# Kernel optimization log

Hardware: AMD Instinct MI355X
Metric: run time of the kernel (lower is better)

## Reference

```python
import jax, jax.numpy as jnp
import numpy as np

NEG = float(-2**32 + 1)  # huge negative used by the original sign-based masking
EPS = 1e-8
NUM_BLOCKS = 3
NUM_HEADS = 1


def _mha(xq, xk, xv, Wq, bq, Wk, bk, Wv, bv):
    # manual QKV with ReLU, as in the torch module
    Q = jax.nn.relu(xq @ Wq + bq)   # [B, Lq, D]
    K = jax.nn.relu(xk @ Wk + bk)   # [B, Lk, D]
    V = jax.nn.relu(xv @ Wv + bv)
    B, Lq, D = Q.shape
    Lk = K.shape[1]
    dh = D // NUM_HEADS
    Qh = Q.reshape(B, Lq, NUM_HEADS, dh)
    Kh = K.reshape(B, Lk, NUM_HEADS, dh)
    Vh = V.reshape(B, Lk, NUM_HEADS, dh)
    scores = jnp.einsum('bqhd,bkhd->bhqk', Qh, Kh) / jnp.sqrt(jnp.float32(dh))
    # sign-based key padding mask (rows whose embedding-sum is exactly 0)
    key_mask0 = (jnp.sign(jnp.abs(jnp.sum(xk, axis=-1))) == 0.0).astype(scores.dtype)  # [B, Lk]
    cond = key_mask0[:, None, None, :]
    scores = NEG * cond + scores * (1.0 - cond)
    attn = jax.nn.softmax(scores, axis=-1)
    # post-softmax query mask
    qmask = jnp.sign(jnp.abs(jnp.sum(xq, axis=-1)))  # [B, Lq]
    attn = attn * qmask[:, None, :, None]
    out = jnp.einsum('bhqk,bkhd->bqhd', attn, Vh).reshape(B, Lq, D)
    return out + xq  # residual; note: the torch mha never applies its layernorm


def _layernorm(x, g, b):
    mu = jnp.mean(x, axis=-1, keepdims=True)
    var = jnp.mean(jnp.square(x - mu), axis=-1, keepdims=True)
    return (x - mu) / jnp.sqrt(var + EPS) * g + b


def _ffn(x, W1, b1, W2, b2, g, bln):
    h = jax.nn.relu(x @ W1 + b1) @ W2 + b2
    return _layernorm(h, g, bln) + x


def setup_inputs() -> dict:
    key = jax.random.key(0)
    ks = jax.random.split(key, 9)
    B, L, V, D, NB = 4096, 50, 50000, 200, NUM_BLOCKS
    tokens = jax.random.randint(ks[0], (B, L), 0, V)
    emb = jax.random.normal(ks[1], (V, D), dtype=jnp.float32) * 0.1
    emb = emb.at[0].set(0.0)  # padding token row -> triggers sign masks
    s = 1.0 / np.sqrt(D)
    Wq = jax.random.normal(ks[2], (NB, D, D), dtype=jnp.float32) * s
    Wk = jax.random.normal(ks[3], (NB, D, D), dtype=jnp.float32) * s
    Wv = jax.random.normal(ks[4], (NB, D, D), dtype=jnp.float32) * s
    W1 = jax.random.normal(ks[5], (NB, D, D), dtype=jnp.float32) * s
    W2 = jax.random.normal(ks[6], (NB, D, D), dtype=jnp.float32) * s
    z = jnp.zeros((NB, D), dtype=jnp.float32)
    return dict(tokens=tokens, emb=emb,
                Wq=Wq, bq=z, Wk=Wk, bk=z, Wv=Wv, bv=z,
                W1=W1, b1=z, W2=W2, b2=z,
                ln_g=jnp.ones((NB, D), dtype=jnp.float32), ln_b=z)


def reference(tokens, emb, Wq, bq, Wk, bk, Wv, bv, W1, b1, W2, b2, ln_g, ln_b):
    x = emb[tokens]  # [B, L, D]
    for i in range(NUM_BLOCKS):
        x = _mha(x, x, x, Wq[i], bq[i], Wk[i], bk[i], Wv[i], bv[i])
        x = _ffn(x, W1[i], b1[i], W2[i], b2[i], ln_g[i], ln_b[i])
    return x
```

## Files before the change

### kernel.cpp

```cpp
#include <hip/hip_runtime.h>
#include <hip/hip_bf16.h>
#include <math.h>

#define LQ 50
#define DD 200
#define NBLK 3
#define NT 512

#define KT 7
#define NTL 14
#define MAT_U (KT * NTL * 128)

#define APS 408
#define VTS 72
#define PS  136
#define SS  66

#define NEGC (-4294967295.0f)
#define SCALE 0.07071067811865475f

typedef __attribute__((ext_vector_type(4))) float f32x4;
typedef __attribute__((ext_vector_type(8))) short s16x8;

__device__ __forceinline__ unsigned short bf16_rne(float x) {
  unsigned u = __float_as_uint(x);
  unsigned r = u + 0x7FFF + ((u >> 16) & 1);
  return (unsigned short)(r >> 16);
}
__device__ __forceinline__ float bf16_f(unsigned short h) {
  return __uint_as_float((unsigned)h << 16);
}

__device__ __forceinline__ void splitf(float x, short& h, short& l) {
  __hip_bfloat16 bh = __float2bfloat16(x);
  float hf = __bfloat162float(bh);
  __hip_bfloat16 bl = __float2bfloat16(x - hf);
  h = (short)__builtin_bit_cast(unsigned short, bh);
  l = (short)__builtin_bit_cast(unsigned short, bl);
}
__device__ __forceinline__ unsigned short bfbits(float x) {
  __hip_bfloat16 bh = __float2bfloat16(x);
  return __builtin_bit_cast(unsigned short, bh);
}
__device__ __forceinline__ float joinf(short h, short l) {
  return __bfloat162float(__builtin_bit_cast(__hip_bfloat16, (unsigned short)h)) +
         __bfloat162float(__builtin_bit_cast(__hip_bfloat16, (unsigned short)l));
}

__device__ __forceinline__ float wave_sum(float v) {
  #pragma unroll
  for (int off = 32; off > 0; off >>= 1) v += __shfl_xor(v, off, 64);
  return v;
}
__device__ __forceinline__ float wave_max(float v) {
  #pragma unroll
  for (int off = 32; off > 0; off >>= 1) v = fmaxf(v, __shfl_xor(v, off, 64));
  return v;
}

__global__ __launch_bounds__(64)
void swizzle_w(const float* __restrict__ Wq, const float* __restrict__ Wk,
               const float* __restrict__ Wv, const float* __restrict__ W1,
               const float* __restrict__ W2, unsigned short* __restrict__ wbuf)
{
  int t = blockIdx.x;
  int nt = t % NTL; t /= NTL;
  int kt = t % KT;  t /= KT;
  int mat = t;
  int layer = mat / 5, which = mat % 5;
  const float* W;
  switch (which) {
    case 0: W = Wq; break;
    case 1: W = Wk; break;
    case 2: W = Wv; break;
    case 3: W = W1; break;
    default: W = W2; break;
  }
  W += (size_t)layer * DD * DD;

  const int l = threadIdx.x;
  const int g = l >> 4, c = l & 15;
  const int n = nt * 16 + c;
  s16x8 vh, vl;
  #pragma unroll
  for (int j = 0; j < 8; ++j) {
    int k = kt * 32 + g * 8 + j;
    float w = (k < DD && n < DD) ? W[k * DD + n] : 0.0f;
    unsigned short h = bf16_rne(w);
    unsigned short lo = bf16_rne(w - bf16_f(h));
    vh[j] = (short)h;
    vl[j] = (short)lo;
  }
  size_t base = ((size_t)(mat * KT * NTL + kt * NTL + nt) * 2) * 512 + l * 8;
  *(s16x8*)(wbuf + base)       = vh;
  *(s16x8*)(wbuf + base + 512) = vl;
}

template <int MODE>
__device__ __forceinline__ void big_matmul(
    const short* __restrict__ srcp, const s16x8* __restrict__ wt,
    const float* __restrict__ bias, short* __restrict__ dstp,
    float* __restrict__ dstf, int wv, int lane)
{
  const int g = lane >> 4, c = lane & 15;
  const int n1 = wv, n2 = wv + 8;
  const bool has2 = (n2 < 13);

  const short* arow[4];
  #pragma unroll
  for (int m = 0; m < 4; ++m) {
    int r = m * 16 + c;
    if (r >= LQ) r = 0;
    arow[m] = srcp + r * APS;
  }

  f32x4 acc0[4], acc1[4];
  #pragma unroll
  for (int m = 0; m < 4; ++m) { acc0[m] = (f32x4)0.f; acc1[m] = (f32x4)0.f; }

  const s16x8* p1 = wt + n1 * 128 + lane;
  s16x8 b1h = p1[0], b1l = p1[64];
  s16x8 b2h = (s16x8)0, b2l = (s16x8)0;
  if (has2) { const s16x8* p2 = wt + n2 * 128 + lane; b2h = p2[0]; b2l = p2[64]; }

  #pragma unroll 1
  for (int kt = 0; kt < KT; ++kt) {
    s16x8 x1h = (s16x8)0, x1l = (s16x8)0, x2h = (s16x8)0, x2l = (s16x8)0;
    if (kt + 1 < KT) {
      const s16x8* q1 = wt + ((kt + 1) * NTL + n1) * 128 + lane;
      x1h = q1[0]; x1l = q1[64];
      if (has2) {
        const s16x8* q2 = wt + ((kt + 1) * NTL + n2) * 128 + lane;
        x2h = q2[0]; x2l = q2[64];
      }
    }
    const int ch = kt * 4 + g;
    s16x8 ah[4], al[4];
    if (ch < 25) {
      #pragma unroll
      for (int m = 0; m < 4; ++m) {
        const short* ap = arow[m] + ch * 16;
        ah[m] = *(const s16x8*)ap;
        al[m] = *(const s16x8*)(ap + 8);
      }
    } else {
      #pragma unroll
      for (int m = 0; m < 4; ++m) { ah[m] = (s16x8)0; al[m] = (s16x8)0; }
    }
    if (MODE == 0) {
      #pragma unroll
      for (int m = 0; m < 4; ++m) {
        acc0[m] = __builtin_amdgcn_mfma_f32_16x16x32_bf16(b1h, ah[m], acc0[m], 0, 0, 0);
        acc0[m] = __builtin_amdgcn_mfma_f32_16x16x32_bf16(b1h, al[m], acc0[m], 0, 0, 0);
        acc0[m] = __builtin_amdgcn_mfma_f32_16x16x32_bf16(b1l, ah[m], acc0[m], 0, 0, 0);
      }
      if (has2) {
        #pragma unroll
        for (int m = 0; m < 4; ++m) {
          acc1[m] = __builtin_amdgcn_mfma_f32_16x16x32_bf16(b2h, ah[m], acc1[m], 0, 0, 0);
          acc1[m] = __builtin_amdgcn_mfma_f32_16x16x32_bf16(b2h, al[m], acc1[m], 0, 0, 0);
          acc1[m] = __builtin_amdgcn_mfma_f32_16x16x32_bf16(b2l, ah[m], acc1[m], 0, 0, 0);
        }
      }
    } else {
      #pragma unroll
      for (int m = 0; m < 4; ++m) {
        acc0[m] = __builtin_amdgcn_mfma_f32_16x16x32_bf16(ah[m], b1h, acc0[m], 0, 0, 0);
        acc0[m] = __builtin_amdgcn_mfma_f32_16x16x32_bf16(al[m], b1h, acc0[m], 0, 0, 0);
        acc0[m] = __builtin_amdgcn_mfma_f32_16x16x32_bf16(ah[m], b1l, acc0[m], 0, 0, 0);
      }
      if (has2) {
        #pragma unroll
        for (int m = 0; m < 4; ++m) {
          acc1[m] = __builtin_amdgcn_mfma_f32_16x16x32_bf16(ah[m], b2h, acc1[m], 0, 0, 0);
          acc1[m] = __builtin_amdgcn_mfma_f32_16x16x32_bf16(al[m], b2h, acc1[m], 0, 0, 0);
          acc1[m] = __builtin_amdgcn_mfma_f32_16x16x32_bf16(ah[m], b2l, acc1[m], 0, 0, 0);
        }
      }
    }
    b1h = x1h; b1l = x1l; b2h = x2h; b2l = x2l;
  }

  if (MODE == 0) {
    #pragma unroll
    for (int t = 0; t < 2; ++t) {
      const int nt = t ? n2 : n1;
      if (nt < 13) {
        const int nb = nt * 16 + g * 4;
        if (nb + 3 < DD) {
          float4 bv = *(const float4*)(bias + nb);
          #pragma unroll
          for (int m = 0; m < 4; ++m) {
            const int r = m * 16 + c;
            if (r < LQ) {
              const f32x4 ac = t ? acc1[m] : acc0[m];
              float v0 = fmaxf(ac[0] + bv.x, 0.f);
              float v1 = fmaxf(ac[1] + bv.y, 0.f);
              float v2 = fmaxf(ac[2] + bv.z, 0.f);
              float v3 = fmaxf(ac[3] + bv.w, 0.f);
              short h0, l0, h1, l1, h2, l2, h3, l3;
              splitf(v0, h0, l0); splitf(v1, h1, l1);
              splitf(v2, h2, l2); splitf(v3, h3, l3);
              uint2 ph, pl;
              ph.x = (unsigned short)h0 | ((unsigned)(unsigned short)h1 << 16);
              ph.y = (unsigned short)h2 | ((unsigned)(unsigned short)h3 << 16);
              pl.x = (unsigned short)l0 | ((unsigned)(unsigned short)l1 << 16);
              pl.y = (unsigned short)l2 | ((unsigned)(unsigned short)l3 << 16);
              short* base = dstp + r * APS + (nb >> 3) * 16 + (nb & 7);
              *(uint2*)base = ph;
              *(uint2*)(base + 8) = pl;
            }
          }
        }
      }
    }
  } else {
    #pragma unroll
    for (int t = 0; t < 2; ++t) {
      const int nt = t ? n2 : n1;
      const int col = nt * 16 + c;
      if (col < DD) {
        const float bv = bias[col];
        #pragma unroll
        for (int m = 0; m < 4; ++m) {
          const int rb = m * 16 + g * 4;
          if (MODE == 1) {
            float vv[4];
            #pragma unroll
            for (int q = 0; q < 4; ++q) {
              const int r = rb + q;
              float v = (t ? acc1[m][q] : acc0[m][q]) + bv;
              vv[q] = (r < LQ) ? fmaxf(v, 0.f) : 0.f;
            }
            unsigned u0 = (unsigned)bfbits(vv[0]) | ((unsigned)bfbits(vv[1]) << 16);
            unsigned u1 = (unsigned)bfbits(vv[2]) | ((unsigned)bfbits(vv[3]) << 16);
            uint2 pk; pk.x = u0; pk.y = u1;
            *(uint2*)(dstp + col * VTS + (rb >> 3) * 8 + (rb & 7)) = pk;
          } else {
            #pragma unroll
            for (int q = 0; q < 4; ++q) {
              const int r = rb + q;
              float v = (t ? acc1[m][q] : acc0[m][q]) + bv;
              if (r < LQ) dstf[r * DD + col] = v;
            }
          }
        }
      }
    }
  }
}

__global__ __launch_bounds__(NT)
void transformer_kernel(const int* __restrict__ tokens,
                        const float* __restrict__ emb,
                        const unsigned short* __restrict__ wbuf,
                        const float* __restrict__ bq, const float* __restrict__ bk,
                        const float* __restrict__ bv, const float* __restrict__ b1,
                        const float* __restrict__ b2,
                        const float* __restrict__ lng, const float* __restrict__ lnb,
                        float* __restrict__ out)
{
  __shared__ __align__(16) short xs_p[LQ * APS];
  __shared__ __align__(16) short q_p [LQ * APS];
  __shared__ __align__(16) short k_p [LQ * APS];
  __shared__ __align__(16) short vt_p[DD * VTS];
  __shared__ float rowsum[52];

  float* Sf   = (float*)q_p;
  short* Pp   = q_p + 8192;
  float* h2f  = (float*)k_p;

  const int b    = blockIdx.x;
  const int tid  = threadIdx.x;
  const int lane = tid & 63;
  const int wv   = tid >> 6;
  const int g    = lane >> 4, c = lane & 15;

  for (int o = tid; o < LQ * 25; o += NT) {
    int r = o / 25, ch = o % 25;
    int tok = tokens[b * LQ + r];
    const float* ep = emb + (size_t)tok * DD + ch * 8;
    float4 a0 = *(const float4*)ep;
    float4 a1 = *(const float4*)(ep + 4);
    float xv[8] = {a0.x, a0.y, a0.z, a0.w, a1.x, a1.y, a1.z, a1.w};
    s16x8 hh, ll;
    #pragma unroll
    for (int j = 0; j < 8; ++j) { short h, l; splitf(xv[j], h, l); hh[j] = h; ll[j] = l; }
    short* dp = xs_p + r * APS + ch * 16;
    *(s16x8*)dp = hh;
    *(s16x8*)(dp + 8) = ll;
  }
  __syncthreads();

  for (int layer = 0; layer < NBLK; ++layer) {
    const s16x8* wq  = (const s16x8*)wbuf + (size_t)(layer * 5 + 0) * MAT_U;
    const s16x8* wk  = (const s16x8*)wbuf + (size_t)(layer * 5 + 1) * MAT_U;
    const s16x8* wvv = (const s16x8*)wbuf + (size_t)(layer * 5 + 2) * MAT_U;
    const s16x8* w1  = (const s16x8*)wbuf + (size_t)(layer * 5 + 3) * MAT_U;
    const s16x8* w2  = (const s16x8*)wbuf + (size_t)(layer * 5 + 4) * MAT_U;
    const float* bql = bq + layer * DD;
    const float* bkl = bk + layer * DD;
    const float* bvl = bv + layer * DD;
    const float* b1l = b1 + layer * DD;
    const float* b2l = b2 + layer * DD;
    const float* gl  = lng + layer * DD;
    const float* bl  = lnb + layer * DD;

    for (int r = wv; r < LQ; r += 8) {
      float s = 0.f;
      #pragma unroll
      for (int t = 0; t < 4; ++t) {
        int cc = lane + 64 * t;
        if (cc < DD) {
          const short* p = xs_p + r * APS + (cc >> 3) * 16 + (cc & 7);
          s += joinf(p[0], p[8]);
        }
      }
      s = wave_sum(s);
      if (lane == 0) rowsum[r] = s;
    }

    big_matmul<0>(xs_p, wq,  bql, q_p,  nullptr, wv, lane);
    big_matmul<0>(xs_p, wk,  bkl, k_p,  nullptr, wv, lane);
    big_matmul<1>(xs_p, wvv, bvl, vt_p, nullptr, wv, lane);
    __syncthreads();

    f32x4 s0 = (f32x4)0.f, s1 = (f32x4)0.f;
    {
      const int mt = wv >> 1;
      const int nk0 = (wv & 1) * 2;
      int qr = mt * 16 + c;         if (qr >= LQ) qr = 0;
      int kj0 = nk0 * 16 + c;       if (kj0 >= LQ) kj0 = 0;
      int kj1 = (nk0 + 1) * 16 + c; if (kj1 >= LQ) kj1 = 0;
      const short* qrow = q_p + qr * APS;
      const short* k0r  = k_p + kj0 * APS;
      const short* k1r  = k_p + kj1 * APS;
      #pragma unroll 1
      for (int kt = 0; kt < KT; ++kt) {
        const int ch = kt * 4 + g;
        s16x8 qh = (s16x8)0, ql = (s16x8)0;
        s16x8 kh0 = (s16x8)0, kl0 = (s16x8)0, kh1 = (s16x8)0, kl1 = (s16x8)0;
        if (ch < 25) {
          qh  = *(const s16x8*)(qrow + ch * 16); ql  = *(const s16x8*)(qrow + ch * 16 + 8);
          kh0 = *(const s16x8*)(k0r + ch * 16);  kl0 = *(const s16x8*)(k0r + ch * 16 + 8);
          kh1 = *(const s16x8*)(k1r + ch * 16);  kl1 = *(const s16x8*)(k1r + ch * 16 + 8);
        }
        s0 = __builtin_amdgcn_mfma_f32_16x16x32_bf16(qh, kh0, s0, 0, 0, 0);
        s0 = __builtin_amdgcn_mfma_f32_16x16x32_bf16(ql, kh0, s0, 0, 0, 0);
        s0 = __builtin_amdgcn_mfma_f32_16x16x32_bf16(qh, kl0, s0, 0, 0, 0);
        s1 = __builtin_amdgcn_mfma_f32_16x16x32_bf16(qh, kh1, s1, 0, 0, 0);
        s1 = __builtin_amdgcn_mfma_f32_16x16x32_bf16(ql, kh1, s1, 0, 0, 0);
        s1 = __builtin_amdgcn_mfma_f32_16x16x32_bf16(qh, kl1, s1, 0, 0, 0);
      }
    }
    __syncthreads();

    {
      const int mt = wv >> 1;
      const int nk0 = (wv & 1) * 2;
      #pragma unroll
      for (int t = 0; t < 2; ++t) {
        const int j = (nk0 + t) * 16 + c;
        const f32x4 sa = t ? s1 : s0;
        const bool km = (j < LQ) && (rowsum[j] != 0.0f);
        #pragma unroll
        for (int q = 0; q < 4; ++q) {
          const int qi = mt * 16 + g * 4 + q;
          if (qi < LQ) Sf[qi * SS + j] = km ? sa[q] * SCALE : NEGC;
        }
      }
    }
    __syncthreads();

    for (int r = wv; r < LQ; r += 8) {
      float sm = -INFINITY;
      if (lane < LQ) sm = Sf[r * SS + lane];
      float m = wave_max(sm);
      float e = (lane < LQ) ? __expf(sm - m) : 0.0f;
      float ssum = wave_sum(e);
      float qm = (rowsum[r] == 0.0f) ? 0.0f : 1.0f;
      float a = e / ssum * qm;
      short h, l; splitf(a, h, l);
      short* pp = Pp + r * PS + (lane >> 3) * 16 + (lane & 7);
      pp[0] = h; pp[8] = l;
    }
    __syncthreads();

    {
      s16x8 pbh[4][2], pbl[4][2];
      #pragma unroll
      for (int nq = 0; nq < 4; ++nq) {
        int pr = nq * 16 + c; if (pr >= LQ) pr = 0;
        const short* pp = Pp + pr * PS;
        #pragma unroll
        for (int kt = 0; kt < 2; ++kt) {
          pbh[nq][kt] = *(const s16x8*)(pp + (kt * 4 + g) * 16);
          pbl[nq][kt] = *(const s16x8*)(pp + (kt * 4 + g) * 16 + 8);
        }
      }
      #pragma unroll
      for (int mi = 0; mi < 2; ++mi) {
        const int mt = wv + 8 * mi;
        if (mt < 13) {
          f32x4 pa[4];
          #pragma unroll
          for (int nq = 0; nq < 4; ++nq) pa[nq] = (f32x4)0.f;
          int vr = mt * 16 + c; if (vr >= DD) vr = 0;
          const short* vrow = vt_p + vr * VTS;
          #pragma unroll
          for (int kt = 0; kt < 2; ++kt) {
            s16x8 vh = *(const s16x8*)(vrow + (kt * 4 + g) * 8);
            #pragma unroll
            for (int nq = 0; nq < 4; ++nq) {
              pa[nq] = __builtin_amdgcn_mfma_f32_16x16x32_bf16(vh, pbh[nq][kt], pa[nq], 0, 0, 0);
              pa[nq] = __builtin_amdgcn_mfma_f32_16x16x32_bf16(vh, pbl[nq][kt], pa[nq], 0, 0, 0);
            }
          }
          const int d0 = mt * 16 + g * 4;
          if (d0 + 3 < DD) {
            #pragma unroll
            for (int nq = 0; nq < 4; ++nq) {
              const int qq = nq * 16 + c;
              if (qq < LQ) {
                short* base = xs_p + qq * APS + (d0 >> 3) * 16 + (d0 & 7);
                uint2 ph = *(const uint2*)base;
                uint2 pl = *(const uint2*)(base + 8);
                float f0 = joinf((short)(ph.x & 0xFFFF), (short)(pl.x & 0xFFFF)) + pa[nq][0];
                float f1 = joinf((short)(ph.x >> 16),    (short)(pl.x >> 16))    + pa[nq][1];
                float f2 = joinf((short)(ph.y & 0xFFFF), (short)(pl.y & 0xFFFF)) + pa[nq][2];
                float f3 = joinf((short)(ph.y >> 16),    (short)(pl.y >> 16))    + pa[nq][3];
                short h0, l0, h1, l1, h2, l2, h3, l3;
                splitf(f0, h0, l0); splitf(f1, h1, l1);
                splitf(f2, h2, l2); splitf(f3, h3, l3);
                ph.x = (unsigned short)h0 | ((unsigned)(unsigned short)h1 << 16);
                ph.y = (unsigned short)h2 | ((unsigned)(unsigned short)h3 << 16);
                pl.x = (unsigned short)l0 | ((unsigned)(unsigned short)l1 << 16);
                pl.y = (unsigned short)l2 | ((unsigned)(unsigned short)l3 << 16);
                *(uint2*)base = ph;
                *(uint2*)(base + 8) = pl;
              }
            }
          }
        }
      }
    }
    __syncthreads();

    big_matmul<0>(xs_p, w1, b1l, q_p, nullptr, wv, lane);
    __syncthreads();
    big_matmul<2>(q_p, w2, b2l, nullptr, h2f, wv, lane);
    __syncthreads();

    for (int r = wv; r < LQ; r += 8) {
      float hv[4];
      #pragma unroll
      for (int t = 0; t < 4; ++t) {
        int cc = lane + 64 * t;
        hv[t] = (cc < DD) ? h2f[r * DD + cc] : 0.f;
      }
      float mu = wave_sum(hv[0] + hv[1] + hv[2] + hv[3]) * (1.0f / 200.0f);
      float d0 = hv[0] - mu, d1 = hv[1] - mu, d2 = hv[2] - mu;
      float d3 = (lane + 192 < DD) ? (hv[3] - mu) : 0.f;
      float var = wave_sum(d0 * d0 + d1 * d1 + d2 * d2 + d3 * d3) * (1.0f / 200.0f);
      float inv = 1.0f / sqrtf(var + 1e-8f);
      float dd4[4] = {d0, d1, d2, d3};
      #pragma unroll
      for (int t = 0; t < 4; ++t) {
        int cc = lane + 64 * t;
        if (cc < DD) {
          short* hp = xs_p + r * APS + (cc >> 3) * 16 + (cc & 7);
          float nv = dd4[t] * inv * gl[cc] + bl[cc] + joinf(hp[0], hp[8]);
          short h, l; splitf(nv, h, l);
          hp[0] = h; hp[8] = l;
        }
      }
    }
    __syncthreads();
  }

  for (int o = tid; o < LQ * 25; o += NT) {
    int r = o / 25, ch = o % 25;
    const short* sp = xs_p + r * APS + ch * 16;
    s16x8 hh = *(const s16x8*)sp;
    s16x8 ll = *(const s16x8*)(sp + 8);
    float4 o0, o1;
    o0.x = joinf(hh[0], ll[0]); o0.y = joinf(hh[1], ll[1]);
    o0.z = joinf(hh[2], ll[2]); o0.w = joinf(hh[3], ll[3]);
    o1.x = joinf(hh[4], ll[4]); o1.y = joinf(hh[5], ll[5]);
    o1.z = joinf(hh[6], ll[6]); o1.w = joinf(hh[7], ll[7]);
    float* op = out + ((size_t)b * LQ + r) * DD + ch * 8;
    *(float4*)op = o0;
    *(float4*)(op + 4) = o1;
  }
}

extern "C" void kernel_launch(void* const* d_in, const int* in_sizes, int n_in,
                              void* d_out, int out_size, void* d_ws, size_t ws_size,
                              hipStream_t stream) {
  const int*   tokens = (const int*)  d_in[0];
  const float* emb    = (const float*)d_in[1];
  const float* Wq     = (const float*)d_in[2];
  const float* bq     = (const float*)d_in[3];
  const float* Wk     = (const float*)d_in[4];
  const float* bk     = (const float*)d_in[5];
  const float* Wv     = (const float*)d_in[6];
  const float* bv     = (const float*)d_in[7];
  const float* W1     = (const float*)d_in[8];
  const float* b1     = (const float*)d_in[9];
  const float* W2     = (const float*)d_in[10];
  const float* b2     = (const float*)d_in[11];
  const float* lng    = (const float*)d_in[12];
  const float* lnb    = (const float*)d_in[13];
  float* out = (float*)d_out;
  unsigned short* wbuf = (unsigned short*)d_ws;

  hipLaunchKernelGGL(swizzle_w, dim3(15 * KT * NTL), dim3(64), 0, stream,
                     Wq, Wk, Wv, W1, W2, wbuf);

  const int B = in_sizes[0] / LQ;
  hipLaunchKernelGGL(transformer_kernel, dim3(B), dim3(NT), 0, stream,
                     tokens, emb, wbuf, bq, bk, bv, b1, b2, lng, lnb, out);
}
```

Baseline: 1.887 ms.

## Double block to 16 waves, giving each wave one output tile

Raises the workgroup from 8 to 16 waves and remaps work so each wave owns a single 16-column tile in the projection matmuls, a single score tile in QK^T, and a single V tile in PV. Row loops for layernorm and softmax now stride by 16 waves. This shortens the per-wave critical path and exposes more parallelism per block. In exchange, 3 of 16 waves sit idle in the matmuls, the weight loads per wave are no longer shared across two tiles, and the larger block may cut blocks per CU or limit registers.

```diff
diff --git a/kernel.cpp b/kernel.cpp
--- a/kernel.cpp
+++ b/kernel.cpp
@@ -5,7 +5,8 @@
 #define LQ 50
 #define DD 200
 #define NBLK 3
-#define NT 512
+#define NT 1024
+#define NW 16
 
 #define KT 7
 #define NTL 14
@@ -102,9 +103,10 @@
     const float* __restrict__ bias, short* __restrict__ dstp,
     float* __restrict__ dstf, int wv, int lane)
 {
+  const bool act = (wv < 13);
+  if (!act) return;
   const int g = lane >> 4, c = lane & 15;
-  const int n1 = wv, n2 = wv + 8;
-  const bool has2 = (n2 < 13);
+  const int n1 = wv;
 
   const short* arow[4];
   #pragma unroll
@@ -114,25 +116,19 @@
     arow[m] = srcp + r * APS;
   }
 
-  f32x4 acc0[4], acc1[4];
+  f32x4 acc0[4];
   #pragma unroll
-  for (int m = 0; m < 4; ++m) { acc0[m] = (f32x4)0.f; acc1[m] = (f32x4)0.f; }
+  for (int m = 0; m < 4; ++m) acc0[m] = (f32x4)0.f;
 
   const s16x8* p1 = wt + n1 * 128 + lane;
   s16x8 b1h = p1[0], b1l = p1[64];
-  s16x8 b2h = (s16x8)0, b2l = (s16x8)0;
-  if (has2) { const s16x8* p2 = wt + n2 * 128 + lane; b2h = p2[0]; b2l = p2[64]; }
 
   #pragma unroll 1
   for (int kt = 0; kt < KT; ++kt) {
-    s16x8 x1h = (s16x8)0, x1l = (s16x8)0, x2h = (s16x8)0, x2l = (s16x8)0;
+    s16x8 x1h = (s16x8)0, x1l = (s16x8)0;
     if (kt + 1 < KT) {
       const s16x8* q1 = wt + ((kt + 1) * NTL + n1) * 128 + lane;
       x1h = q1[0]; x1l = q1[64];
-      if (has2) {
-        const s16x8* q2 = wt + ((kt + 1) * NTL + n2) * 128 + lane;
-        x2h = q2[0]; x2l = q2[64];
-      }
     }
     const int ch = kt * 4 + g;
     s16x8 ah[4], al[4];
@@ -154,14 +150,6 @@
         acc0[m] = __builtin_amdgcn_mfma_f32_16x16x32_bf16(b1h, al[m], acc0[m], 0, 0, 0);
         acc0[m] = __builtin_amdgcn_mfma_f32_16x16x32_bf16(b1l, ah[m], acc0[m], 0, 0, 0);
       }
-      if (has2) {
-        #pragma unroll
-        for (int m = 0; m < 4; ++m) {
-          acc1[m] = __builtin_amdgcn_mfma_f32_16x16x32_bf16(b2h, ah[m], acc1[m], 0, 0, 0);
-          acc1[m] = __builtin_amdgcn_mfma_f32_16x16x32_bf16(b2h, al[m], acc1[m], 0, 0, 0);
-          acc1[m] = __builtin_amdgcn_mfma_f32_16x16x32_bf16(b2l, ah[m], acc1[m], 0, 0, 0);
-        }
-      }
     } else {
       #pragma unroll
       for (int m = 0; m < 4; ++m) {
@@ -169,80 +157,62 @@
         acc0[m] = __builtin_amdgcn_mfma_f32_16x16x32_bf16(al[m], b1h, acc0[m], 0, 0, 0);
         acc0[m] = __builtin_amdgcn_mfma_f32_16x16x32_bf16(ah[m], b1l, acc0[m], 0, 0, 0);
       }
-      if (has2) {
-        #pragma unroll
-        for (int m = 0; m < 4; ++m) {
-          acc1[m] = __builtin_amdgcn_mfma_f32_16x16x32_bf16(ah[m], b2h, acc1[m], 0, 0, 0);
-          acc1[m] = __builtin_amdgcn_mfma_f32_16x16x32_bf16(al[m], b2h, acc1[m], 0, 0, 0);
-          acc1[m] = __builtin_amdgcn_mfma_f32_16x16x32_bf16(ah[m], b2l, acc1[m], 0, 0, 0);
-        }
-      }
-    }
-    b1h = x1h; b1l = x1l; b2h = x2h; b2l = x2l;
+    }
+    b1h = x1h; b1l = x1l;
   }
 
   if (MODE == 0) {
-    #pragma unroll
-    for (int t = 0; t < 2; ++t) {
-      const int nt = t ? n2 : n1;
-      if (nt < 13) {
-        const int nb = nt * 16 + g * 4;
-        if (nb + 3 < DD) {
-          float4 bv = *(const float4*)(bias + nb);
+    const int nb = n1 * 16 + g * 4;
+    if (nb + 3 < DD) {
+      float4 bv = *(const float4*)(bias + nb);
+      #pragma unroll
+      for (int m = 0; m < 4; ++m) {
+        const int r = m * 16 + c;
+        if (r < LQ) {
+          const f32x4 ac = acc0[m];
+          float v0 = fmaxf(ac[0] + bv.x, 0.f);
+          float v1 = fmaxf(ac[1] + bv.y, 0.f);
+          float v2 = fmaxf(ac[2] + bv.z, 0.f);
+          float v3 = fmaxf(ac[3] + bv.w, 0.f);
+          short h0, l0, h1, l1, h2, l2, h3, l3;
+          splitf(v0, h0, l0); splitf(v1, h1, l1);
+          splitf(v2, h2, l2); splitf(v3, h3, l3);
+          uint2 ph, pl;
+          ph.x = (unsigned short)h0 | ((unsigned)(unsigned short)h1 << 16);
+          ph.y = (unsigned short)h2 | ((unsigned)(unsigned short)h3 << 16);
+          pl.x = (unsigned short)l0 | ((unsigned)(unsigned short)l1 << 16);
+          pl.y = (unsigned short)l2 | ((unsigned)(unsigned short)l3 << 16);
+          short* base = dstp + r * APS + (nb >> 3) * 16 + (nb & 7);
+          *(uint2*)base = ph;
+          *(uint2*)(base + 8) = pl;
+        }
+      }
+    }
+  } else {
+    const int col = n1 * 16 + c;
+    if (col < DD) {
+      const float bv = bias[col];
+      #pragma unroll
+      for (int m = 0; m < 4; ++m) {
+        const int rb = m * 16 + g * 4;
+        if (MODE == 1) {
+          float vv[4];
           #pragma unroll
-          for (int m = 0; m < 4; ++m) {
-            const int r = m * 16 + c;
-            if (r < LQ) {
-              const f32x4 ac = t ? acc1[m] : acc0[m];
-              float v0 = fmaxf(ac[0] + bv.x, 0.f);
-              float v1 = fmaxf(ac[1] + bv.y, 0.f);
-              float v2 = fmaxf(ac[2] + bv.z, 0.f);
-              float v3 = fmaxf(ac[3] + bv.w, 0.f);
-              short h0, l0, h1, l1, h2, l2, h3, l3;
-              splitf(v0, h0, l0); splitf(v1, h1, l1);
-              splitf(v2, h2, l2); splitf(v3, h3, l3);
-              uint2 ph, pl;
-              ph.x = (unsigned short)h0 | ((unsigned)(unsigned short)h1 << 16);
-              ph.y = (unsigned short)h2 | ((unsigned)(unsigned short)h3 << 16);
-              pl.x = (unsigned short)l0 | ((unsigned)(unsigned short)l1 << 16);
-              pl.y = (unsigned short)l2 | ((unsigned)(unsigned short)l3 << 16);
-              short* base = dstp + r * APS + (nb >> 3) * 16 + (nb & 7);
-              *(uint2*)base = ph;
-              *(uint2*)(base + 8) = pl;
-            }
+          for (int q = 0; q < 4; ++q) {
+            const int r = rb + q;
+            float v = acc0[m][q] + bv;
+            vv[q] = (r < LQ) ? fmaxf(v, 0.f) : 0.f;
           }
-        }
-      }
-    }
-  } else {
-    #pragma unroll
-    for (int t = 0; t < 2; ++t) {
-      const int nt = t ? n2 : n1;
-      const int col = nt * 16 + c;
-      if (col < DD) {
-        const float bv = bias[col];
-        #pragma unroll
-        for (int m = 0; m < 4; ++m) {
-          const int rb = m * 16 + g * 4;
-          if (MODE == 1) {
-            float vv[4];
-            #pragma unroll
-            for (int q = 0; q < 4; ++q) {
-              const int r = rb + q;
-              float v = (t ? acc1[m][q] : acc0[m][q]) + bv;
-              vv[q] = (r < LQ) ? fmaxf(v, 0.f) : 0.f;
-            }
-            unsigned u0 = (unsigned)bfbits(vv[0]) | ((unsigned)bfbits(vv[1]) << 16);
-            unsigned u1 = (unsigned)bfbits(vv[2]) | ((unsigned)bfbits(vv[3]) << 16);
-            uint2 pk; pk.x = u0; pk.y = u1;
-            *(uint2*)(dstp + col * VTS + (rb >> 3) * 8 + (rb & 7)) = pk;
-          } else {
-            #pragma unroll
-            for (int q = 0; q < 4; ++q) {
-              const int r = rb + q;
-              float v = (t ? acc1[m][q] : acc0[m][q]) + bv;
-              if (r < LQ) dstf[r * DD + col] = v;
-            }
+          unsigned u0 = (unsigned)bfbits(vv[0]) | ((unsigned)bfbits(vv[1]) << 16);
+          unsigned u1 = (unsigned)bfbits(vv[2]) | ((unsigned)bfbits(vv[3]) << 16);
+          uint2 pk; pk.x = u0; pk.y = u1;
+          *(uint2*)(dstp + col * VTS + (rb >> 3) * 8 + (rb & 7)) = pk;
+        } else {
+          #pragma unroll
+          for (int q = 0; q < 4; ++q) {
+            const int r = rb + q;
+            float v = acc0[m][q] + bv;
+            if (r < LQ) dstf[r * DD + col] = v;
           }
         }
       }
@@ -306,7 +276,7 @@
     const float* gl  = lng + layer * DD;
     const float* bl  = lnb + layer * DD;
 
-    for (int r = wv; r < LQ; r += 8) {
+    for (int r = wv; r < LQ; r += NW) {
       float s = 0.f;
       #pragma unroll
       for (int t = 0; t < 4; ++t) {
@@ -325,54 +295,44 @@
     big_matmul<1>(xs_p, wvv, bvl, vt_p, nullptr, wv, lane);
     __syncthreads();
 
-    f32x4 s0 = (f32x4)0.f, s1 = (f32x4)0.f;
+    f32x4 s0 = (f32x4)0.f;
     {
-      const int mt = wv >> 1;
-      const int nk0 = (wv & 1) * 2;
-      int qr = mt * 16 + c;         if (qr >= LQ) qr = 0;
-      int kj0 = nk0 * 16 + c;       if (kj0 >= LQ) kj0 = 0;
-      int kj1 = (nk0 + 1) * 16 + c; if (kj1 >= LQ) kj1 = 0;
+      const int mt  = wv >> 2;
+      const int ntk = wv & 3;
+      int qr = mt * 16 + c;   if (qr >= LQ) qr = 0;
+      int kj = ntk * 16 + c;  if (kj >= LQ) kj = 0;
       const short* qrow = q_p + qr * APS;
-      const short* k0r  = k_p + kj0 * APS;
-      const short* k1r  = k_p + kj1 * APS;
+      const short* k0r  = k_p + kj * APS;
       #pragma unroll 1
       for (int kt = 0; kt < KT; ++kt) {
         const int ch = kt * 4 + g;
         s16x8 qh = (s16x8)0, ql = (s16x8)0;
-        s16x8 kh0 = (s16x8)0, kl0 = (s16x8)0, kh1 = (s16x8)0, kl1 = (s16x8)0;
+        s16x8 kh0 = (s16x8)0, kl0 = (s16x8)0;
         if (ch < 25) {
           qh  = *(const s16x8*)(qrow + ch * 16); ql  = *(const s16x8*)(qrow + ch * 16 + 8);
           kh0 = *(const s16x8*)(k0r + ch * 16);  kl0 = *(const s16x8*)(k0r + ch * 16 + 8);
-          kh1 = *(const s16x8*)(k1r + ch * 16);  kl1 = *(const s16x8*)(k1r + ch * 16 + 8);
         }
         s0 = __builtin_amdgcn_mfma_f32_16x16x32_bf16(qh, kh0, s0, 0, 0, 0);
         s0 = __builtin_amdgcn_mfma_f32_16x16x32_bf16(ql, kh0, s0, 0, 0, 0);
         s0 = __builtin_amdgcn_mfma_f32_16x16x32_bf16(qh, kl0, s0, 0, 0, 0);
-        s1 = __builtin_amdgcn_mfma_f32_16x16x32_bf16(qh, kh1, s1, 0, 0, 0);
-        s1 = __builtin_amdgcn_mfma_f32_16x16x32_bf16(ql, kh1, s1, 0, 0, 0);
-        s1 = __builtin_amdgcn_mfma_f32_16x16x32_bf16(qh, kl1, s1, 0, 0, 0);
       }
     }
     __syncthreads();
 
     {
-      const int mt = wv >> 1;
-      const int nk0 = (wv & 1) * 2;
-      #pragma unroll
-      for (int t = 0; t < 2; ++t) {
-        const int j = (nk0 + t) * 16 + c;
-        const f32x4 sa = t ? s1 : s0;
-        const bool km = (j < LQ) && (rowsum[j] != 0.0f);
-        #pragma unroll
-        for (int q = 0; q < 4; ++q) {
-          const int qi = mt * 16 + g * 4 + q;
-          if (qi < LQ) Sf[qi * SS + j] = km ? sa[q] * SCALE : NEGC;
-        }
-      }
-    }
-    __syncthreads();
-
-    for (int r = wv; r < LQ; r += 8) {
+      const int mt  = wv >> 2;
+      const int ntk = wv & 3;
+      const int j = ntk * 16 + c;
+      const bool km = (j < LQ) && (rowsum[j] != 0.0f);
+      #pragma unroll
+      for (int q = 0; q < 4; ++q) {
+        const int qi = mt * 16 + g * 4 + q;
+        if (qi < LQ && j < 64) Sf[qi * SS + j] = km ? s0[q] * SCALE : NEGC;
+      }
+    }
+    __syncthreads();
+
+    for (int r = wv; r < LQ; r += NW) {
       float sm = -INFINITY;
       if (lane < LQ) sm = Sf[r * SS + lane];
       float m = wave_max(sm);
@@ -386,7 +346,7 @@
     }
     __syncthreads();
 
-    {
+    if (wv < 13) {
       s16x8 pbh[4][2], pbl[4][2];
       #pragma unroll
       for (int nq = 0; nq < 4; ++nq) {
@@ -398,49 +358,44 @@
           pbl[nq][kt] = *(const s16x8*)(pp + (kt * 4 + g) * 16 + 8);
         }
       }
-      #pragma unroll
-      for (int mi = 0; mi < 2; ++mi) {
-        const int mt = wv + 8 * mi;
-        if (mt < 13) {
-          f32x4 pa[4];
-          #pragma unroll
-          for (int nq = 0; nq < 4; ++nq) pa[nq] = (f32x4)0.f;
-          int vr = mt * 16 + c; if (vr >= DD) vr = 0;
-          const short* vrow = vt_p + vr * VTS;
-          #pragma unroll
-          for (int kt = 0; kt < 2; ++kt) {
-            s16x8 vh = *(const s16x8*)(vrow + (kt * 4 + g) * 8);
-            #pragma unroll
-            for (int nq = 0; nq < 4; ++nq) {
-              pa[nq] = __builtin_amdgcn_mfma_f32_16x16x32_bf16(vh, pbh[nq][kt], pa[nq], 0, 0, 0);
-              pa[nq] = __builtin_amdgcn_mfma_f32_16x16x32_bf16(vh, pbl[nq][kt], pa[nq], 0, 0, 0);
-            }
+      const int mt = wv;
+      f32x4 pa[4];
+      #pragma unroll
+      for (int nq = 0; nq < 4; ++nq) pa[nq] = (f32x4)0.f;
+      int vr = mt * 16 + c; if (vr >= DD) vr = 0;
+      const short* vrow = vt_p + vr * VTS;
+      #pragma unroll
+      for (int kt = 0; kt < 2; ++kt) {
+        s16x8 vh = *(const s16x8*)(vrow + (kt * 4 + g) * 8);
+        #pragma unroll
+        for (int nq = 0; nq < 4; ++nq) {
+          pa[nq] = __builtin_amdgcn_mfma_f32_16x16x32_bf16(vh, pbh[nq][kt], pa[nq], 0, 0, 0);
+          pa[nq] = __builtin_amdgcn_mfma_f32_16x16x32_bf16(vh, pbl[nq][kt], pa[nq], 0, 0, 0);
+        }
+      }
+      const int d0 = mt * 16 + g * 4;
+      if (d0 + 3 < DD) {
+        #pragma unroll
+        for (int nq = 0; nq < 4; ++nq) {
+          const int qq = nq * 16 + c;
+          if (qq < LQ) {
+            short* base = xs_p + qq * APS + (d0 >> 3) * 16 + (d0 & 7);
+            uint2 ph = *(const uint2*)base;
+            uint2 pl = *(const uint2*)(base + 8);
+            float f0 = joinf((short)(ph.x & 0xFFFF), (short)(pl.x & 0xFFFF)) + pa[nq][0];
+            float f1 = joinf((short)(ph.x >> 16),    (short)(pl.x >> 16))    + pa[nq][1];
+            float f2 = joinf((short)(ph.y & 0xFFFF), (short)(pl.y & 0xFFFF)) + pa[nq][2];
+            float f3 = joinf((short)(ph.y >> 16),    (short)(pl.y >> 16))    + pa[nq][3];
+            short h0, l0, h1, l1, h2, l2, h3, l3;
+            splitf(f0, h0, l0); splitf(f1, h1, l1);
+            splitf(f2, h2, l2); splitf(f3, h3, l3);
+            ph.x = (unsigned short)h0 | ((unsigned)(unsigned short)h1 << 16);
+            ph.y = (unsigned short)h2 | ((unsigned)(unsigned short)h3 << 16);
+            pl.x = (unsigned short)l0 | ((unsigned)(unsigned short)l1 << 16);
+            pl.y = (unsigned short)l2 | ((unsigned)(unsigned short)l3 << 16);
+            *(uint2*)base = ph;
+            *(uint2*)(base + 8) = pl;
           }
-          const int d0 = mt * 16 + g * 4;
-          if (d0 + 3 < DD) {
-            #pragma unroll
-            for (int nq = 0; nq < 4; ++nq) {
-              const int qq = nq * 16 + c;
-              if (qq < LQ) {
-                short* base = xs_p + qq * APS + (d0 >> 3) * 16 + (d0 & 7);
-                uint2 ph = *(const uint2*)base;
-                uint2 pl = *(const uint2*)(base + 8);
-                float f0 = joinf((short)(ph.x & 0xFFFF), (short)(pl.x & 0xFFFF)) + pa[nq][0];
-                float f1 = joinf((short)(ph.x >> 16),    (short)(pl.x >> 16))    + pa[nq][1];
-                float f2 = joinf((short)(ph.y & 0xFFFF), (short)(pl.y & 0xFFFF)) + pa[nq][2];
-                float f3 = joinf((short)(ph.y >> 16),    (short)(pl.y >> 16))    + pa[nq][3];
-                short h0, l0, h1, l1, h2, l2, h3, l3;
-                splitf(f0, h0, l0); splitf(f1, h1, l1);
-                splitf(f2, h2, l2); splitf(f3, h3, l3);
-                ph.x = (unsigned short)h0 | ((unsigned)(unsigned short)h1 << 16);
-                ph.y = (unsigned short)h2 | ((unsigned)(unsigned short)h3 << 16);
-                pl.x = (unsigned short)l0 | ((unsigned)(unsigned short)l1 << 16);
-                pl.y = (unsigned short)l2 | ((unsigned)(unsigned short)l3 << 16);
-                *(uint2*)base = ph;
-                *(uint2*)(base + 8) = pl;
-              }
-            }
-          }
         }
       }
     }
@@ -451,7 +406,7 @@
     big_matmul<2>(q_p, w2, b2l, nullptr, h2f, wv, lane);
     __syncthreads();
 
-    for (int r = wv; r < LQ; r += 8) {
+    for (int r = wv; r < LQ; r += NW) {
       float hv[4];
       #pragma unroll
       for (int t = 0; t < 4; ++t) {
```

Result: faster. 1.678 ms (-11.1%).
